# Kernel optimization log

Measured on AMD Instinct MI355X. Metric: run time of the kernel, lower is better.

## Reference

```python
import jax, jax.numpy as jnp
import numpy as np

B, T, C = 2, 2048, 1024
H = 16
HS = C // H  # head_size = 64


def setup_inputs() -> dict:
    key = jax.random.key(0)
    k1, k2, k3 = jax.random.split(key, 3)
    x = jax.random.normal(k1, (B, T, C), dtype=jnp.float32)
    # nn.Linear(n_embd, 3*n_embd): weight [3C, C], bias [3C]
    W = jax.random.normal(k2, (3 * C, C), dtype=jnp.float32) * (C ** -0.5)
    b = jax.random.normal(k3, (3 * C,), dtype=jnp.float32) * 0.02
    return {"x": x, "W": W, "b": b}


def reference(x, W, b):
    Bs, Ts, Cs = x.shape
    # fused QKV projection: [B,T,3C]
    qkv = x @ W.T + b
    qkv = qkv.reshape(Bs, Ts, 3, H, HS)
    q, k, v = jnp.moveaxis(qkv, 2, 0)          # each [B,T,H,HS]
    q = q.transpose(0, 2, 1, 3)                 # [B,H,T,HS]
    k = k.transpose(0, 2, 1, 3)
    v = v.transpose(0, 2, 1, 3)
    scale = HS ** -0.5
    wei = jnp.einsum('bhqd,bhkd->bhqk', q, k) * scale  # [B,H,T,T]
    causal = jnp.tril(jnp.ones((Ts, Ts), dtype=bool))
    wei = jnp.where(causal, wei, -jnp.inf)
    wei = jax.nn.softmax(wei, axis=-1)
    out = jnp.einsum('bhqk,bhkd->bhqd', wei, v)        # [B,H,T,HS]
    return out.transpose(0, 2, 1, 3).reshape(Bs, Ts, Cs)
```

## Files before the change

### kernel.cpp

```cpp
#include <hip/hip_runtime.h>
#include <hip/hip_bf16.h>

typedef __attribute__((ext_vector_type(8))) short bf16x8;
typedef __attribute__((ext_vector_type(4))) float f32x4;

#define BATCH 2
#define T_SEQ 2048
#define C_EMB 1024
#define NH 16
#define HS 64

__device__ __forceinline__ void gld_lds16(const __hip_bfloat16* g, void* l) {
    __builtin_amdgcn_global_load_lds((const __attribute__((address_space(1))) uint32_t*)g,
                                     (__attribute__((address_space(3))) uint32_t*)l, 16, 0, 0);
}

__device__ __forceinline__ unsigned pk_bf16(float a, float b) {
    unsigned r;
    asm("v_cvt_pk_bf16_f32 %0, %1, %2" : "=v"(r) : "v"(a), "v"(b));
    return r;
}

__device__ __forceinline__ void pack_store(char* dst, float4 a, float4 b) {
    uint4 u;
    u.x = pk_bf16(a.x, a.y);
    u.y = pk_bf16(a.z, a.w);
    u.z = pk_bf16(b.x, b.y);
    u.w = pk_bf16(b.z, b.w);
    *(uint4*)dst = u;
}

#define NT_K 16

__launch_bounds__(512, 2)
__global__ void qkv_gemm(const float* __restrict__ xf,
                         const float* __restrict__ wf,
                         const float* __restrict__ bias,
                         __hip_bfloat16* __restrict__ qo,
                         __hip_bfloat16* __restrict__ ko,
                         __hip_bfloat16* __restrict__ vto)
{
    __shared__ __align__(16) char smem[114688];
    __hip_bfloat16* ASB = (__hip_bfloat16*)smem;
    __hip_bfloat16* BSB = (__hip_bfloat16*)(smem + 65536);
    const int nTn = (3 * C_EMB) / 192;
    int bid = blockIdx.x;
    int wgid = (bid & 7) * 32 + (bid >> 3);
    int bm = wgid / nTn, bn = wgid % nTn;
    int m0 = bm * 256, n0 = bn * 192;
    int tid  = threadIdx.x;
    int lane = tid & 63, w = tid >> 6;
    int wr = w >> 1, wc = w & 1;
    int c = lane & 15, g = lane >> 4;
    int sr = lane >> 2;
    int j  = lane & 3;
    int pc = j ^ ((sr >> 1) & 3);
    int rchnk = (g ^ ((c >> 1) & 3)) << 4;

#define LOAD_AB(kt, kh, pa_, pb_) { \
    int col_ = (kt) * 64 + (kh) * 32 + j * 8; \
    _Pragma("unroll") for (int i_ = 0; i_ < 2; ++i_) { \
        const float* s_ = &xf[(size_t)(m0 + w * 32 + i_ * 16 + sr) * 1024 + col_]; \
        pa_[2 * i_] = *(const float4*)s_; pa_[2 * i_ + 1] = *(const float4*)(s_ + 4); } \
    if (w < 4) { \
        _Pragma("unroll") for (int i_ = 0; i_ < 2; ++i_) { \
            const float* s_ = &wf[(size_t)(n0 + w * 32 + i_ * 16 + sr) * 1024 + col_]; \
            pb_[2 * i_] = *(const float4*)s_; pb_[2 * i_ + 1] = *(const float4*)(s_ + 4); } \
    } else { \
        const float* s_ = &wf[(size_t)(n0 + 128 + (w - 4) * 16 + sr) * 1024 + col_]; \
        pb_[0] = *(const float4*)s_; pb_[1] = *(const float4*)(s_ + 4); } }

#define WRITE_AB(tb_, pa_, pb_) { \
    _Pragma("unroll") for (int i_ = 0; i_ < 2; ++i_) \
        pack_store((char*)&ASB[(tb_) * 8192 + (w * 32 + i_ * 16 + sr) * 32 + pc * 8], \
                   pa_[2 * i_], pa_[2 * i_ + 1]); \
    if (w < 4) { \
        _Pragma("unroll") for (int i_ = 0; i_ < 2; ++i_) \
            pack_store((char*)&BSB[(tb_) * 6144 + (w * 32 + i_ * 16 + sr) * 32 + pc * 8], \
                       pb_[2 * i_], pb_[2 * i_ + 1]); \
    } else { \
        pack_store((char*)&BSB[(tb_) * 6144 + (128 + (w - 4) * 16 + sr) * 32 + pc * 8], \
                   pb_[0], pb_[1]); } }

    f32x4 acc[4][6];
#pragma unroll
    for (int mi = 0; mi < 4; ++mi)
#pragma unroll
        for (int ni = 0; ni < 6; ++ni)
            acc[mi][ni] = (f32x4){0.f, 0.f, 0.f, 0.f};

    float4 s0a[4], s0b[4], s1a[4], s1b[4];
    int tb_s0 = 0, tb_s1 = 0;
    bool v_s0 = false, v_s1 = false;

    LOAD_AB(0, 0, s0a, s0b); WRITE_AB(0, s0a, s0b);
    LOAD_AB(0, 1, s0a, s0b); WRITE_AB(1, s0a, s0b);
    LOAD_AB(1, 0, s1a, s1b); tb_s1 = 2; v_s1 = true;
    __syncthreads();

    for (int t = 0; t < NT_K; ++t) {
        int buf = t & 1;
#pragma unroll
        for (int ks = 0; ks < 2; ++ks) {
            const __hip_bfloat16* AL = &ASB[(buf * 2 + ks) * 8192];
            const __hip_bfloat16* BL = &BSB[(buf * 2 + ks) * 6144];
            bf16x8 bfr[6], af[4];
#pragma unroll
            for (int ni = 0; ni < 6; ++ni)
                bfr[ni] = *(const bf16x8*)((const char*)BL + (wc * 96 + ni * 16 + c) * 64 + rchnk);
#pragma unroll
            for (int mi = 0; mi < 4; ++mi)
                af[mi] = *(const bf16x8*)((const char*)AL + (wr * 64 + mi * 16 + c) * 64 + rchnk);
            if (ks == 0) {
                if (t + 1 < NT_K) { LOAD_AB(t + 1, 1, s0a, s0b); tb_s0 = ((t + 1) & 1) * 2 + 1; v_s0 = true; }
                else v_s0 = false;
            } else {
                if (t + 2 < NT_K) { LOAD_AB(t + 2, 0, s1a, s1b); tb_s1 = ((t + 2) & 1) * 2; v_s1 = true; }
                else v_s1 = false;
            }
            __builtin_amdgcn_s_setprio(1);
#pragma unroll
            for (int mi = 0; mi < 4; ++mi)
#pragma unroll
                for (int ni = 0; ni < 6; ++ni)
                    acc[mi][ni] = __builtin_amdgcn_mfma_f32_16x16x32_bf16(af[mi], bfr[ni], acc[mi][ni], 0, 0, 0);
            __builtin_amdgcn_s_setprio(0);
            if (ks == 0) { if (v_s1) WRITE_AB(tb_s1, s1a, s1b); }
            else         { if (v_s0) WRITE_AB(tb_s0, s0a, s0b); }
            asm volatile("s_waitcnt lgkmcnt(0)" ::: "memory");
            __builtin_amdgcn_s_barrier();
        }
    }
#undef LOAD_AB
#undef WRITE_AB

    const float QSCALE = 0.125f * 1.44269504088896340736f;
    __syncthreads();
    int b = m0 >> 11;
    int t0 = (m0 & (T_SEQ - 1)) + wr * 64;
#pragma unroll
    for (int ni = 0; ni < 6; ++ni) {
        int nb = n0 + wc * 96 + ni * 16;
        int s = nb >> 10;
        int h = (nb >> 6) & (NH - 1);
        float bv = bias[nb + c];
        if (s < 2) {
            __hip_bfloat16* dst = (s == 0) ? qo : ko;
            float scale = (s == 0) ? QSCALE : 1.0f;
            int dd = (nb & 63) + c;
            size_t bhb = (size_t)(b * NH + h) * T_SEQ;
#pragma unroll
            for (int mi = 0; mi < 4; ++mi) {
#pragma unroll
                for (int r = 0; r < 4; ++r) {
                    int tt = t0 + mi * 16 + g * 4 + r;
                    dst[(bhb + tt) * HS + dd] = __float2bfloat16((acc[mi][ni][r] + bv) * scale);
                }
            }
        } else {
            int dbase = nb & 63;
            char* scr = smem + (w * 6 + ni) * 2048;
#pragma unroll
            for (int mi = 0; mi < 4; ++mi) {
#pragma unroll
                for (int r = 0; r < 4; ++r) {
                    int m = mi * 16 + g * 4 + r;
                    __hip_bfloat16 hv = __float2bfloat16(acc[mi][ni][r] + bv);
                    *(ushort*)(scr + c * 128 + ((((m >> 3) ^ (c & 7)) & 7) << 4) + (m & 7) * 2) = *(ushort*)&hv;
                }
            }
            size_t bhv = (size_t)(b * NH + h);
            int d_lo = lane >> 3, tch = lane & 7;
#pragma unroll
            for (int p = 0; p < 2; ++p) {
                int d = p * 8 + d_lo;
                bf16x8 vv = *(bf16x8*)(scr + d * 128 + (((tch ^ (d & 7)) & 7) << 4));
                *(bf16x8*)(&vto[(bhv * HS + dbase + d) * T_SEQ + t0 + tch * 8]) = vv;
            }
        }
    }
}

__launch_bounds__(256, 4)
__global__ void attn_fwd(const __hip_bfloat16* __restrict__ qb,
                         const __hip_bfloat16* __restrict__ kb,
                         const __hip_bfloat16* __restrict__ vtb,
                         float* __restrict__ out)
{
    __shared__ __align__(16) char smem[40960];

    int idx = blockIdx.x;
    int bh = idx & 31;
    int qt = 31 - (idx >> 5);
    int w  = threadIdx.x >> 6;
    int lane = threadIdx.x & 63;
    int c = lane & 15, g = lane >> 4;
    char* p_strip = smem + 32768 + w * 2048;

    const __hip_bfloat16* Qp = qb  + (size_t)bh * T_SEQ * HS;
    const __hip_bfloat16* Kp = kb  + (size_t)bh * T_SEQ * HS;
    const __hip_bfloat16* Vp = vtb + (size_t)bh * HS * T_SEQ;
    int b = bh >> 4, h = bh & (NH - 1);

    int srow = lane >> 3;
    int scol = ((lane & 7) ^ srow) << 3;
    int swz  = (c & 7) << 4;
    int krow0 = w * 16 + srow;
    int krow1 = w * 16 + 8 + srow;
    int qw = qt * 64 + w * 16;
    int ntile = qt + 1;

    bf16x8 qf[2];
    qf[0] = *(const bf16x8*)(&Qp[(size_t)(qw + c) * HS + g * 8]);
    qf[1] = *(const bf16x8*)(&Qp[(size_t)(qw + c) * HS + 32 + g * 8]);

    f32x4 oacc[4];
#pragma unroll
    for (int i = 0; i < 4; ++i) oacc[i] = (f32x4){0.f, 0.f, 0.f, 0.f};
    float lrow = 0.f;

#define ATT_STAGE(t_, buf_) { \
    int k0_ = (t_) * 64; \
    char* kb_ = smem + (buf_) * 8192; \
    char* vb_ = smem + 16384 + (buf_) * 8192; \
    gld_lds16(&Kp[(size_t)(k0_ + krow0) * HS + scol],  kb_ + (w * 16) * 128); \
    gld_lds16(&Kp[(size_t)(k0_ + krow1) * HS + scol],  kb_ + (w * 16 + 8) * 128); \
    gld_lds16(&Vp[(size_t)krow0 * T_SEQ + k0_ + scol], vb_ + (w * 16) * 128); \
    gld_lds16(&Vp[(size_t)krow1 * T_SEQ + k0_ + scol], vb_ + (w * 16 + 8) * 128); }

    ATT_STAGE(0, 0);

    for (int tix = 0; tix < ntile; ++tix) {
        int cur = tix & 1;
        asm volatile("s_waitcnt vmcnt(0)" ::: "memory");
        __builtin_amdgcn_s_barrier();
        if (tix + 1 < ntile) ATT_STAGE(tix + 1, cur ^ 1);

        bool diag = (tix == ntile - 1);
        const char* KL = smem + cur * 8192;
        const char* VL = smem + 16384 + cur * 8192;

        f32x4 sacc[4];
#pragma unroll
        for (int i = 0; i < 4; ++i) sacc[i] = (f32x4){0.f, 0.f, 0.f, 0.f};
        __builtin_amdgcn_s_setprio(1);
#pragma unroll
        for (int ks = 0; ks < 2; ++ks)
#pragma unroll
            for (int kc = 0; kc < 4; ++kc)
                if (!diag || kc <= w) {
                    int rr = kc * 16 + c;
                    int colB = (ks * 64 + g * 16) ^ swz;
                    bf16x8 kf = *(const bf16x8*)(KL + rr * 128 + colB);
                    sacc[kc] = __builtin_amdgcn_mfma_f32_16x16x32_bf16(kf, qf[ks], sacc[kc], 0, 0, 0);
                }
        __builtin_amdgcn_s_setprio(0);

#pragma unroll
        for (int kc = 0; kc < 4; ++kc) {
            float p0, p1, p2, p3;
            if (!diag) {
                p0 = __builtin_amdgcn_exp2f(sacc[kc][0]);
                p1 = __builtin_amdgcn_exp2f(sacc[kc][1]);
                p2 = __builtin_amdgcn_exp2f(sacc[kc][2]);
                p3 = __builtin_amdgcn_exp2f(sacc[kc][3]);
            } else {
                int kbase = kc * 16 + g * 4;
                int lim = w * 16 + c;
                p0 = (kc <= w && kbase + 0 <= lim) ? __builtin_amdgcn_exp2f(sacc[kc][0]) : 0.f;
                p1 = (kc <= w && kbase + 1 <= lim) ? __builtin_amdgcn_exp2f(sacc[kc][1]) : 0.f;
                p2 = (kc <= w && kbase + 2 <= lim) ? __builtin_amdgcn_exp2f(sacc[kc][2]) : 0.f;
                p3 = (kc <= w && kbase + 3 <= lim) ? __builtin_amdgcn_exp2f(sacc[kc][3]) : 0.f;
            }
            lrow += (p0 + p1) + (p2 + p3);
            unsigned lo = pk_bf16(p0, p1);
            unsigned hi = pk_bf16(p2, p3);
            int gran = ((kc * 2 + (g >> 1)) ^ (c & 7)) << 4;
            *(uint2*)(p_strip + c * 128 + gran + ((g & 1) << 3)) = make_uint2(lo, hi);
        }

        int ksm = diag ? ((w >= 2) ? 2 : 1) : 2;
        __builtin_amdgcn_s_setprio(1);
#pragma unroll
        for (int ks = 0; ks < 2; ++ks) {
            if (ks >= ksm) break;
            int pgran = ((ks * 4 + g) ^ (c & 7)) << 4;
            bf16x8 pf = *(bf16x8*)(p_strip + c * 128 + pgran);
#pragma unroll
            for (int d16 = 0; d16 < 4; ++d16) {
                int dr = d16 * 16 + c;
                int colB = (ks * 64 + g * 16) ^ swz;
                bf16x8 vf = *(const bf16x8*)(VL + dr * 128 + colB);
                oacc[d16] = __builtin_amdgcn_mfma_f32_16x16x32_bf16(vf, pf, oacc[d16], 0, 0, 0);
            }
        }
        __builtin_amdgcn_s_setprio(0);
    }

    float v = lrow;
    v += __shfl_xor(v, 16, 64);
    v += __shfl_xor(v, 32, 64);
    float linv = 1.0f / v;
    float* orow = &out[((size_t)(b * T_SEQ + qw + c)) * C_EMB + h * HS + g * 4];
#pragma unroll
    for (int d16 = 0; d16 < 4; ++d16) {
        float4 st;
        st.x = oacc[d16][0] * linv;
        st.y = oacc[d16][1] * linv;
        st.z = oacc[d16][2] * linv;
        st.w = oacc[d16][3] * linv;
        *(float4*)(&orow[d16 * 16]) = st;
    }
#undef ATT_STAGE
}

extern "C" void kernel_launch(void* const* d_in, const int* in_sizes, int n_in,
                              void* d_out, int out_size, void* d_ws, size_t ws_size,
                              hipStream_t stream) {
    const float* x    = (const float*)d_in[0];
    const float* W    = (const float*)d_in[1];
    const float* bias = (const float*)d_in[2];
    float* out = (float*)d_out;

    char* ws = (char*)d_ws;
    __hip_bfloat16* qo  = (__hip_bfloat16*)(ws + (14u << 20));
    __hip_bfloat16* ko  = (__hip_bfloat16*)(ws + (22u << 20));
    __hip_bfloat16* vto = (__hip_bfloat16*)(ws + (30u << 20));

    int gemm_grid = (BATCH * T_SEQ / 256) * (3 * C_EMB / 192);
    qkv_gemm<<<gemm_grid, 512, 0, stream>>>(x, W, bias, qo, ko, vto);

    attn_fwd<<<1024, 256, 0, stream>>>(qo, ko, vto, out);
}
```

Measured before the change: 71.71 us.

## Halve QKV GEMM N-tile and shrink LDS staging for higher occupancy

Shrinks the QKV projection GEMM output tile from 256x192 to 256x96 and doubles the grid to 512 blocks. LDS staging drops from a double-buffered pair of k-halves to a single set, which lowers shared memory to 44KB, and the launch-bounds occupancy hint rises from 2 to 4. The aim is more resident workgroups and better CU coverage to hide latency. In exchange the A tile of x is re-read by twice as many blocks, each block does less MFMA work per LDS read, and the tighter register budget may cause spills. The V transpose scratch now reuses one 2KB slot per wave, which relies on the write and read of each column slice staying inside the same wave.

```diff
diff --git a/kernel.cpp b/kernel.cpp
--- a/kernel.cpp
+++ b/kernel.cpp
@@ -32,7 +32,7 @@
 
 #define NT_K 16
 
-__launch_bounds__(512, 2)
+__launch_bounds__(512, 4)
 __global__ void qkv_gemm(const float* __restrict__ xf,
                          const float* __restrict__ wf,
                          const float* __restrict__ bias,
@@ -40,14 +40,14 @@
                          __hip_bfloat16* __restrict__ ko,
                          __hip_bfloat16* __restrict__ vto)
 {
-    __shared__ __align__(16) char smem[114688];
+    __shared__ __align__(16) char smem[45056];
     __hip_bfloat16* ASB = (__hip_bfloat16*)smem;
-    __hip_bfloat16* BSB = (__hip_bfloat16*)(smem + 65536);
-    const int nTn = (3 * C_EMB) / 192;
+    __hip_bfloat16* BSB = (__hip_bfloat16*)(smem + 32768);
+    const int nTn = (3 * C_EMB) / 96;
     int bid = blockIdx.x;
-    int wgid = (bid & 7) * 32 + (bid >> 3);
+    int wgid = (bid & 7) * 64 + (bid >> 3);
     int bm = wgid / nTn, bn = wgid % nTn;
-    int m0 = bm * 256, n0 = bn * 192;
+    int m0 = bm * 256, n0 = bn * 96;
     int tid  = threadIdx.x;
     int lane = tid & 63, w = tid >> 6;
     int wr = w >> 1, wc = w & 1;
@@ -62,71 +62,61 @@
     _Pragma("unroll") for (int i_ = 0; i_ < 2; ++i_) { \
         const float* s_ = &xf[(size_t)(m0 + w * 32 + i_ * 16 + sr) * 1024 + col_]; \
         pa_[2 * i_] = *(const float4*)s_; pa_[2 * i_ + 1] = *(const float4*)(s_ + 4); } \
-    if (w < 4) { \
-        _Pragma("unroll") for (int i_ = 0; i_ < 2; ++i_) { \
-            const float* s_ = &wf[(size_t)(n0 + w * 32 + i_ * 16 + sr) * 1024 + col_]; \
-            pb_[2 * i_] = *(const float4*)s_; pb_[2 * i_ + 1] = *(const float4*)(s_ + 4); } \
-    } else { \
-        const float* s_ = &wf[(size_t)(n0 + 128 + (w - 4) * 16 + sr) * 1024 + col_]; \
+    if (w < 6) { \
+        const float* s_ = &wf[(size_t)(n0 + w * 16 + sr) * 1024 + col_]; \
         pb_[0] = *(const float4*)s_; pb_[1] = *(const float4*)(s_ + 4); } }
 
-#define WRITE_AB(tb_, pa_, pb_) { \
+#define WRITE_AB(buf_, pa_, pb_) { \
     _Pragma("unroll") for (int i_ = 0; i_ < 2; ++i_) \
-        pack_store((char*)&ASB[(tb_) * 8192 + (w * 32 + i_ * 16 + sr) * 32 + pc * 8], \
+        pack_store((char*)&ASB[(buf_) * 8192 + (w * 32 + i_ * 16 + sr) * 32 + pc * 8], \
                    pa_[2 * i_], pa_[2 * i_ + 1]); \
-    if (w < 4) { \
-        _Pragma("unroll") for (int i_ = 0; i_ < 2; ++i_) \
-            pack_store((char*)&BSB[(tb_) * 6144 + (w * 32 + i_ * 16 + sr) * 32 + pc * 8], \
-                       pb_[2 * i_], pb_[2 * i_ + 1]); \
-    } else { \
-        pack_store((char*)&BSB[(tb_) * 6144 + (128 + (w - 4) * 16 + sr) * 32 + pc * 8], \
-                   pb_[0], pb_[1]); } }
-
-    f32x4 acc[4][6];
+    if (w < 6) \
+        pack_store((char*)&BSB[(buf_) * 3072 + (w * 16 + sr) * 32 + pc * 8], \
+                   pb_[0], pb_[1]); }
+
+    f32x4 acc[4][3];
 #pragma unroll
     for (int mi = 0; mi < 4; ++mi)
 #pragma unroll
-        for (int ni = 0; ni < 6; ++ni)
+        for (int ni = 0; ni < 3; ++ni)
             acc[mi][ni] = (f32x4){0.f, 0.f, 0.f, 0.f};
 
-    float4 s0a[4], s0b[4], s1a[4], s1b[4];
-    int tb_s0 = 0, tb_s1 = 0;
+    float4 s0a[4], s1a[4];
+    float4 s0b[2], s1b[2];
     bool v_s0 = false, v_s1 = false;
 
     LOAD_AB(0, 0, s0a, s0b); WRITE_AB(0, s0a, s0b);
-    LOAD_AB(0, 1, s0a, s0b); WRITE_AB(1, s0a, s0b);
-    LOAD_AB(1, 0, s1a, s1b); tb_s1 = 2; v_s1 = true;
+    LOAD_AB(0, 1, s1a, s1b); v_s1 = true;
     __syncthreads();
 
     for (int t = 0; t < NT_K; ++t) {
-        int buf = t & 1;
 #pragma unroll
         for (int ks = 0; ks < 2; ++ks) {
-            const __hip_bfloat16* AL = &ASB[(buf * 2 + ks) * 8192];
-            const __hip_bfloat16* BL = &BSB[(buf * 2 + ks) * 6144];
-            bf16x8 bfr[6], af[4];
-#pragma unroll
-            for (int ni = 0; ni < 6; ++ni)
-                bfr[ni] = *(const bf16x8*)((const char*)BL + (wc * 96 + ni * 16 + c) * 64 + rchnk);
+            const __hip_bfloat16* AL = &ASB[ks * 8192];
+            const __hip_bfloat16* BL = &BSB[ks * 3072];
+            bf16x8 bfr[3], af[4];
+#pragma unroll
+            for (int ni = 0; ni < 3; ++ni)
+                bfr[ni] = *(const bf16x8*)((const char*)BL + (wc * 48 + ni * 16 + c) * 64 + rchnk);
 #pragma unroll
             for (int mi = 0; mi < 4; ++mi)
                 af[mi] = *(const bf16x8*)((const char*)AL + (wr * 64 + mi * 16 + c) * 64 + rchnk);
             if (ks == 0) {
-                if (t + 1 < NT_K) { LOAD_AB(t + 1, 1, s0a, s0b); tb_s0 = ((t + 1) & 1) * 2 + 1; v_s0 = true; }
+                if (t + 1 < NT_K) { LOAD_AB(t + 1, 0, s0a, s0b); v_s0 = true; }
                 else v_s0 = false;
             } else {
-                if (t + 2 < NT_K) { LOAD_AB(t + 2, 0, s1a, s1b); tb_s1 = ((t + 2) & 1) * 2; v_s1 = true; }
+                if (t + 1 < NT_K) { LOAD_AB(t + 1, 1, s1a, s1b); v_s1 = true; }
                 else v_s1 = false;
             }
             __builtin_amdgcn_s_setprio(1);
 #pragma unroll
             for (int mi = 0; mi < 4; ++mi)
 #pragma unroll
-                for (int ni = 0; ni < 6; ++ni)
+                for (int ni = 0; ni < 3; ++ni)
                     acc[mi][ni] = __builtin_amdgcn_mfma_f32_16x16x32_bf16(af[mi], bfr[ni], acc[mi][ni], 0, 0, 0);
             __builtin_amdgcn_s_setprio(0);
-            if (ks == 0) { if (v_s1) WRITE_AB(tb_s1, s1a, s1b); }
-            else         { if (v_s0) WRITE_AB(tb_s0, s0a, s0b); }
+            if (ks == 0) { if (v_s1) WRITE_AB(1, s1a, s1b); }
+            else         { if (v_s0) WRITE_AB(0, s0a, s0b); }
             asm volatile("s_waitcnt lgkmcnt(0)" ::: "memory");
             __builtin_amdgcn_s_barrier();
         }
@@ -139,8 +129,8 @@
     int b = m0 >> 11;
     int t0 = (m0 & (T_SEQ - 1)) + wr * 64;
 #pragma unroll
-    for (int ni = 0; ni < 6; ++ni) {
-        int nb = n0 + wc * 96 + ni * 16;
+    for (int ni = 0; ni < 3; ++ni) {
+        int nb = n0 + wc * 48 + ni * 16;
         int s = nb >> 10;
         int h = (nb >> 6) & (NH - 1);
         float bv = bias[nb + c];
@@ -159,7 +149,7 @@
             }
         } else {
             int dbase = nb & 63;
-            char* scr = smem + (w * 6 + ni) * 2048;
+            char* scr = smem + w * 2048;
 #pragma unroll
             for (int mi = 0; mi < 4; ++mi) {
 #pragma unroll
@@ -327,7 +317,7 @@
     __hip_bfloat16* ko  = (__hip_bfloat16*)(ws + (22u << 20));
     __hip_bfloat16* vto = (__hip_bfloat16*)(ws + (30u << 20));
 
-    int gemm_grid = (BATCH * T_SEQ / 256) * (3 * C_EMB / 192);
+    int gemm_grid = (BATCH * T_SEQ / 256) * (3 * C_EMB / 96);
     qkv_gemm<<<gemm_grid, 512, 0, stream>>>(x, W, bias, qo, ko, vto);
 
     attn_fwd<<<1024, 256, 0, stream>>>(qo, ko, vto, out);
```

Result: slower. 126.3 us (+76.1%).
